# Kernel tuning notes

Measured on AMD Instinct MI355X. Metric: run time of the kernel, lower is better.

The kernel has to match this reference:

```python
import jax, jax.numpy as jnp
from jax import lax
import numpy as np

K = 3  # kernel size for both convs


def setup_inputs() -> dict:
    key = jax.random.key(0)
    k1, k2, k3, k4, k5 = jax.random.split(key, 5)
    x = jax.random.normal(k1, (8, 3, 384, 384), dtype=jnp.float32)
    # offset-producing conv: 18 = 2*3*3 offset channels for a 3x3 deform kernel
    w1 = jax.random.normal(k2, (18, 3, K, K), dtype=jnp.float32) * 0.05
    b1 = jax.random.normal(k3, (18,), dtype=jnp.float32) * 0.05
    # deformable conv weight/bias: in=3, out=3, 3x3
    w2 = jax.random.normal(k4, (3, 3, K, K), dtype=jnp.float32) * 0.2
    b2 = jax.random.normal(k5, (3,), dtype=jnp.float32) * 0.05
    return {"x": x, "w1": w1, "b1": b1, "w2": w2, "b2": b2}


def _deform_conv2d(x, offset, w, b):
    # x: [B,C,H,W], offset: [B, 2*K*K, Ho, Wo] (per-tap (dy,dx) interleaved),
    # w: [Co,C,K,K], b: [Co]. stride=1, pad=0, dilation=1, zero-padding bilinear.
    B, C, H, W = x.shape
    KK = K * K
    Ho, Wo = H - (K - 1), W - (K - 1)
    off = offset.reshape(B, KK, 2, Ho, Wo)
    dy, dx = off[:, :, 0], off[:, :, 1]                      # [B,KK,Ho,Wo]

    kh = jnp.repeat(jnp.arange(K, dtype=jnp.float32), K)     # [KK] kernel row
    kw = jnp.tile(jnp.arange(K, dtype=jnp.float32), K)       # [KK] kernel col
    base_y = jnp.arange(Ho, dtype=jnp.float32)[None, :, None] + kh[:, None, None]  # [KK,Ho,1]
    base_x = jnp.arange(Wo, dtype=jnp.float32)[None, None, :] + kw[:, None, None]  # [KK,1,Wo]
    py = base_y[None] + dy                                   # [B,KK,Ho,Wo]
    px = base_x[None] + dx

    y0 = jnp.floor(py)
    x0 = jnp.floor(px)
    wy = py - y0
    wx = px - x0

    x_flat = x.reshape(B, C, H * W)
    N = KK * Ho * Wo

    def gather_corner(yc, xc, wgt):
        valid = (yc >= 0) & (yc <= H - 1) & (xc >= 0) & (xc <= W - 1)
        yi = jnp.clip(yc, 0, H - 1).astype(jnp.int32)
        xi = jnp.clip(xc, 0, W - 1).astype(jnp.int32)
        idx = (yi * W + xi).reshape(B, 1, N)
        g = jnp.take_along_axis(x_flat, idx, axis=2)          # [B,C,N]
        return g * (wgt * valid.astype(x.dtype)).reshape(B, 1, N)

    val = gather_corner(y0, x0, (1 - wy) * (1 - wx))
    val = val + gather_corner(y0, x0 + 1, (1 - wy) * wx)
    val = val + gather_corner(y0 + 1, x0, wy * (1 - wx))
    val = val + gather_corner(y0 + 1, x0 + 1, wy * wx)
    val = val.reshape(B, C, KK, Ho, Wo)

    out = jnp.einsum('bckhw,ock->bohw', val, w.reshape(w.shape[0], C, KK))
    return out + b[None, :, None, None]


def reference(x, w1, b1, w2, b2):
    offset = lax.conv_general_dilated(
        x, w1, window_strides=(1, 1), padding='VALID',
        dimension_numbers=('NCHW', 'OIHW', 'NCHW')) + b1[None, :, None, None]
    return _deform_conv2d(x, offset, w2, b2)
```

## Files before the change

### kernel.cpp

```cpp
#include <hip/hip_runtime.h>


#define BB 8
#define HH 384
#define WW 384
#define HO 382
#define WO 382
#define HW (HH * WW)
#define TW 32
#define TH 8
#define TILES_X 12
#define TILES_Y 48
#define SROWS 15
#define SCOLS 39
#define SSTRIDE 39

typedef float v2f __attribute__((ext_vector_type(2), aligned(4)));
typedef float v4f __attribute__((ext_vector_type(4), aligned(16)));

static __device__ __forceinline__ v2f fma2(v2f a, v2f b, v2f c) {
    return __builtin_elementwise_fma(a, b, c);
}
static __device__ __forceinline__ v4f fma4(v4f a, v4f b, v4f c) {
    return __builtin_elementwise_fma(a, b, c);
}

__global__ __launch_bounds__(256) void deform_tiled(
    const float* __restrict__ x,
    const float* __restrict__ w1,
    const float* __restrict__ b1,
    const float* __restrict__ w2,
    const float* __restrict__ b2,
    float* __restrict__ out)
{
    __shared__ v4f  s_tile[SROWS * SSTRIDE];
    __shared__ float s_w1p[486];
    __shared__ float s_b1[18];
    __shared__ float s_w2p[54];
    __shared__ float s_w2s[27];
    __shared__ float s_b2[3];

    for (int i = threadIdx.x; i < 486; i += 256) {
        const int oc = i / 27, rem = i % 27, c = rem / 9, j = rem % 9;
        const int k = oc >> 1, comp = oc & 1;
        s_w1p[((j * 3 + c) * 9 + k) * 2 + comp] = w1[i];
    }
    if (threadIdx.x < 81) {
        const int i = threadIdx.x;
        const int o = i / 27, c = (i % 27) / 9, k = i % 9;
        if (o < 2) s_w2p[(k * 3 + c) * 2 + o] = w2[i];
        else       s_w2s[k * 3 + c] = w2[i];
    }
    if (threadIdx.x < 18) s_b1[threadIdx.x] = b1[threadIdx.x];
    if (threadIdx.x < 3)  s_b2[threadIdx.x] = b2[threadIdx.x];

    const int b  = blockIdx.x & 7;
    const int t  = blockIdx.x >> 3;
    const int tx = t % TILES_X;
    const int ty = t / TILES_X;
    const int w0 = tx * TW;
    const int r0 = ty * TH;

    const float* xp0 = x + (long)b * 3 * HW;
    const float* xp1 = xp0 + HW;
    const float* xp2 = xp0 + 2 * HW;

    const int gr0 = r0 - 2, gc0 = w0 - 2;
    for (int s = threadIdx.x; s < SROWS * SCOLS; s += 256) {
        const int sr = s / SCOLS, sc = s - sr * SCOLS;
        const int gy = min(max(gr0 + sr, 0), HH - 1);
        const int gx = min(max(gc0 + sc, 0), WW - 1);
        const int base = gy * WW + gx;
        v4f v;
        v.x = xp0[base];
        v.y = xp1[base];
        v.z = xp2[base];
        v.w = 0.f;
        s_tile[sr * SSTRIDE + sc] = v;
    }
    __syncthreads();

    const int wo_in = threadIdx.x & 31;
    const int ho_in = threadIdx.x >> 5;
    const int wo = w0 + wo_in;
    const int ho = r0 + ho_in;
    if (wo >= WO || ho >= HO) return;

    v2f off2[9];
#pragma unroll
    for (int k = 0; k < 9; ++k) {
        v2f v; v.x = s_b1[2 * k]; v.y = s_b1[2 * k + 1];
        off2[k] = v;
    }

    const v2f* w1p = (const v2f*)s_w1p;
#pragma unroll
    for (int j = 0; j < 9; ++j) {
        const int i = j / 3, jj = j % 3;
        const v4f q = s_tile[(ho_in + 2 + i) * SSTRIDE + (wo_in + 2 + jj)];
#pragma unroll
        for (int c = 0; c < 3; ++c) {
            const float xc = (c == 0) ? q.x : (c == 1) ? q.y : q.z;
            v2f xcv; xcv.x = xc; xcv.y = xc;
            const v2f* wrow = w1p + (j * 3 + c) * 9;
#pragma unroll
            for (int k = 0; k < 9; ++k)
                off2[k] = fma2(xcv, wrow[k], off2[k]);
        }
    }

    float acc0 = s_b2[0], acc1 = s_b2[1], acc2 = s_b2[2];
    const v2f* w2p = (const v2f*)s_w2p;

    const bool interior = (gr0 >= 0) & (gc0 >= 0) &
                          (gr0 + SROWS <= HH) & (gc0 + SCOLS <= WW);

    if (interior) {
        unsigned bad = 0u;
#pragma unroll
        for (int k = 0; k < 9; ++k) {
            const int kh = k / 3, kw = k - kh * 3;
            v2f pos; pos.x = (float)(ho + kh); pos.y = (float)(wo + kw);
            pos += off2[k];
            const v2f fl = __builtin_elementwise_floor(pos);
            const v2f fr = pos - fl;
            const int y0 = (int)fl.x;
            const int x0 = (int)fl.y;
            const int ly0 = y0 - gr0;
            const int lx  = x0 - gc0;

            bad |= (((unsigned)ly0 > (unsigned)(SROWS - 2)) |
                    ((unsigned)lx  > (unsigned)(SCOLS - 2))) ? (1u << k) : 0u;

            const float g00 = (1.f - fr.x) * (1.f - fr.y);
            const float g01 = (1.f - fr.x) * fr.y;
            const float g10 = fr.x * (1.f - fr.y);
            const float g11 = fr.x * fr.y;

            const int cy0 = min(max(ly0, 0), SROWS - 2);
            const int cx  = min(max(lx, 0),  SCOLS - 2);
            const v4f* p0 = s_tile + cy0 * SSTRIDE + cx;
            const v4f* p1 = p0 + SSTRIDE;
            const v4f q00 = p0[0], q01 = p0[1];
            const v4f q10 = p1[0], q11 = p1[1];

            v4f gv; gv.x = g00; gv.y = g00; gv.z = g00; gv.w = g00;
            v4f t4 = gv * q00;
            gv.x = g01; gv.y = g01; gv.z = g01; gv.w = g01;
            t4 = fma4(gv, q01, t4);
            gv.x = g10; gv.y = g10; gv.z = g10; gv.w = g10;
            t4 = fma4(gv, q10, t4);
            gv.x = g11; gv.y = g11; gv.z = g11; gv.w = g11;
            t4 = fma4(gv, q11, t4);

            const float v0 = t4.x, v1 = t4.y, v2v = t4.z;

            v2f acc01; acc01.x = acc0; acc01.y = acc1;
            v2f vv;
            vv.x = v0;  vv.y = v0;  acc01 = fma2(vv, w2p[k * 3 + 0], acc01);
            vv.x = v1;  vv.y = v1;  acc01 = fma2(vv, w2p[k * 3 + 1], acc01);
            vv.x = v2v; vv.y = v2v; acc01 = fma2(vv, w2p[k * 3 + 2], acc01);
            acc0 = acc01.x; acc1 = acc01.y;
            acc2 = fmaf(s_w2s[k * 3 + 0], v0, acc2);
            acc2 = fmaf(s_w2s[k * 3 + 1], v1, acc2);
            acc2 = fmaf(s_w2s[k * 3 + 2], v2v, acc2);
        }

        if (bad) {
#pragma unroll 1
            for (int k = 0; k < 9; ++k) {
                if ((bad >> k) & 1u) {
                    const int kh = k / 3, kw = k - kh * 3;
                    v2f pos; pos.x = (float)(ho + kh); pos.y = (float)(wo + kw);
                    pos += off2[k];
                    const v2f fl = __builtin_elementwise_floor(pos);
                    const v2f fr = pos - fl;
                    const int y0 = (int)fl.x;
                    const int x0 = (int)fl.y;

                    const int ly0 = y0 - gr0;
                    const int lx  = x0 - gc0;
                    const float a00 = (1.f - fr.x) * (1.f - fr.y);
                    const float a01 = (1.f - fr.x) * fr.y;
                    const float a10 = fr.x * (1.f - fr.y);
                    const float a11 = fr.x * fr.y;
                    const int cy0 = min(max(ly0, 0), SROWS - 2);
                    const int cx  = min(max(lx, 0),  SCOLS - 2);
                    const v4f* p0 = s_tile + cy0 * SSTRIDE + cx;
                    const v4f* p1 = p0 + SSTRIDE;
                    const v4f w00v = p0[0], w01v = p0[1];
                    const v4f w10v = p1[0], w11v = p1[1];
                    v4f gv; gv.x = a00; gv.y = a00; gv.z = a00; gv.w = a00;
                    v4f tw = gv * w00v;
                    gv.x = a01; gv.y = a01; gv.z = a01; gv.w = a01;
                    tw = fma4(gv, w01v, tw);
                    gv.x = a10; gv.y = a10; gv.z = a10; gv.w = a10;
                    tw = fma4(gv, w10v, tw);
                    gv.x = a11; gv.y = a11; gv.z = a11; gv.w = a11;
                    tw = fma4(gv, w11v, tw);

                    const int ry0 = min(max(y0, 0), HH - 1);
                    const int ry1 = min(max(y0 + 1, 0), HH - 1);
                    const int xbs = min(max(x0, 0), WW - 2);
                    const bool vy0 = (y0 >= 0) & (y0 <= HH - 1);
                    const bool vy1 = (y0 >= -1) & (y0 <= HH - 2);
                    const bool vx0 = (x0 >= 0) & (x0 <= WW - 1);
                    const bool vx1 = (x0 >= -1) & (x0 <= WW - 2);
                    const float wy0m = vy0 ? (1.f - fr.x) : 0.f;
                    const float wy1m = vy1 ? fr.x : 0.f;
                    const float wx0m = vx0 ? (1.f - fr.y) : 0.f;
                    const float wx1m = vx1 ? fr.y : 0.f;
                    const bool selA = (x0 >= WW - 1);
                    const bool selB = (x0 >= 0);
                    const float e0 = (selA ? 0.f : wx0m) + (selB ? 0.f : wx1m);
                    const float e1 = (selA ? wx0m : 0.f) + (selB ? wx1m : 0.f);
                    const float g00 = wy0m * e0, g01 = wy0m * e1;
                    const float g10 = wy1m * e0, g11 = wy1m * e1;
                    const int o0 = ry0 * WW + xbs;
                    const int o1 = ry1 * WW + xbs;
                    v4f q00, q01, q10, q11;
                    q00.x = xp0[o0];     q00.y = xp1[o0];     q00.z = xp2[o0];     q00.w = 0.f;
                    q01.x = xp0[o0 + 1]; q01.y = xp1[o0 + 1]; q01.z = xp2[o0 + 1]; q01.w = 0.f;
                    q10.x = xp0[o1];     q10.y = xp1[o1];     q10.z = xp2[o1];     q10.w = 0.f;
                    q11.x = xp0[o1 + 1]; q11.y = xp1[o1 + 1]; q11.z = xp2[o1 + 1]; q11.w = 0.f;
                    gv.x = g00; gv.y = g00; gv.z = g00; gv.w = g00;
                    v4f tr = gv * q00;
                    gv.x = g01; gv.y = g01; gv.z = g01; gv.w = g01;
                    tr = fma4(gv, q01, tr);
                    gv.x = g10; gv.y = g10; gv.z = g10; gv.w = g10;
                    tr = fma4(gv, q10, tr);
                    gv.x = g11; gv.y = g11; gv.z = g11; gv.w = g11;
                    tr = fma4(gv, q11, tr);

                    const float d0 = tr.x - tw.x;
                    const float d1 = tr.y - tw.y;
                    const float d2 = tr.z - tw.z;

                    v2f acc01; acc01.x = acc0; acc01.y = acc1;
                    v2f vv;
                    vv.x = d0; vv.y = d0; acc01 = fma2(vv, w2p[k * 3 + 0], acc01);
                    vv.x = d1; vv.y = d1; acc01 = fma2(vv, w2p[k * 3 + 1], acc01);
                    vv.x = d2; vv.y = d2; acc01 = fma2(vv, w2p[k * 3 + 2], acc01);
                    acc0 = acc01.x; acc1 = acc01.y;
                    acc2 = fmaf(s_w2s[k * 3 + 0], d0, acc2);
                    acc2 = fmaf(s_w2s[k * 3 + 1], d1, acc2);
                    acc2 = fmaf(s_w2s[k * 3 + 2], d2, acc2);
                }
            }
        }
    } else {
#pragma unroll 1
        for (int k = 0; k < 9; ++k) {
            const int kh = k / 3, kw = k - kh * 3;
            v2f pos; pos.x = (float)(ho + kh); pos.y = (float)(wo + kw);
            pos += off2[k];
            const v2f fl = __builtin_elementwise_floor(pos);
            const v2f fr = pos - fl;
            const int y0 = (int)fl.x;
            const int x0 = (int)fl.y;

            const int ry0 = min(max(y0, 0), HH - 1);
            const int ry1 = min(max(y0 + 1, 0), HH - 1);
            const int xbs = min(max(x0, 0), WW - 2);

            const bool vy0 = (y0 >= 0) & (y0 <= HH - 1);
            const bool vy1 = (y0 >= -1) & (y0 <= HH - 2);
            const bool vx0 = (x0 >= 0) & (x0 <= WW - 1);
            const bool vx1 = (x0 >= -1) & (x0 <= WW - 2);
            const float wy0m = vy0 ? (1.f - fr.x) : 0.f;
            const float wy1m = vy1 ? fr.x : 0.f;
            const float wx0m = vx0 ? (1.f - fr.y) : 0.f;
            const float wx1m = vx1 ? fr.y : 0.f;

            const bool selA = (x0 >= WW - 1);
            const bool selB = (x0 >= 0);
            const float e0 = (selA ? 0.f : wx0m) + (selB ? 0.f : wx1m);
            const float e1 = (selA ? wx0m : 0.f) + (selB ? wx1m : 0.f);
            const float g00 = wy0m * e0, g01 = wy0m * e1;
            const float g10 = wy1m * e0, g11 = wy1m * e1;

            const int ly0 = ry0 - gr0;
            const int ly1 = ry1 - gr0;
            const int lx  = xbs - gc0;
            const bool inTile = ((unsigned)ly0 <= SROWS - 1) &
                                ((unsigned)ly1 <= SROWS - 1) &
                                ((unsigned)lx  <= SCOLS - 2);

            const int cy0 = min(max(ly0, 0), SROWS - 1);
            const int cy1 = min(max(ly1, 0), SROWS - 1);
            const int cx  = min(max(lx, 0),  SCOLS - 2);
            const v4f* p0 = s_tile + cy0 * SSTRIDE + cx;
            const v4f* p1 = s_tile + cy1 * SSTRIDE + cx;
            v4f q00 = p0[0], q01 = p0[1];
            v4f q10 = p1[0], q11 = p1[1];

            if (!inTile) {
                const int o0 = ry0 * WW + xbs;
                const int o1 = ry1 * WW + xbs;
                q00.x = xp0[o0];     q00.y = xp1[o0];     q00.z = xp2[o0];
                q01.x = xp0[o0 + 1]; q01.y = xp1[o0 + 1]; q01.z = xp2[o0 + 1];
                q10.x = xp0[o1];     q10.y = xp1[o1];     q10.z = xp2[o1];
                q11.x = xp0[o1 + 1]; q11.y = xp1[o1 + 1]; q11.z = xp2[o1 + 1];
            }

            v4f gv; gv.x = g00; gv.y = g00; gv.z = g00; gv.w = g00;
            v4f t4 = gv * q00;
            gv.x = g01; gv.y = g01; gv.z = g01; gv.w = g01;
            t4 = fma4(gv, q01, t4);
            gv.x = g10; gv.y = g10; gv.z = g10; gv.w = g10;
            t4 = fma4(gv, q10, t4);
            gv.x = g11; gv.y = g11; gv.z = g11; gv.w = g11;
            t4 = fma4(gv, q11, t4);

            const float v0 = t4.x, v1 = t4.y, v2v = t4.z;

            v2f acc01; acc01.x = acc0; acc01.y = acc1;
            v2f vv;
            vv.x = v0;  vv.y = v0;  acc01 = fma2(vv, w2p[k * 3 + 0], acc01);
            vv.x = v1;  vv.y = v1;  acc01 = fma2(vv, w2p[k * 3 + 1], acc01);
            vv.x = v2v; vv.y = v2v; acc01 = fma2(vv, w2p[k * 3 + 2], acc01);
            acc0 = acc01.x; acc1 = acc01.y;
            acc2 = fmaf(s_w2s[k * 3 + 0], v0, acc2);
            acc2 = fmaf(s_w2s[k * 3 + 1], v1, acc2);
            acc2 = fmaf(s_w2s[k * 3 + 2], v2v, acc2);
        }
    }

    const long obase = ((long)(b * 3) * HO + ho) * WO + wo;
    __builtin_nontemporal_store(acc0, out + obase);
    __builtin_nontemporal_store(acc1, out + obase + (long)HO * WO);
    __builtin_nontemporal_store(acc2, out + obase + 2L * HO * WO);
}

extern "C" void kernel_launch(void* const* d_in, const int* in_sizes, int n_in,
                              void* d_out, int out_size, void* d_ws, size_t ws_size,
                              hipStream_t stream) {
    const float* x  = (const float*)d_in[0];
    const float* w1 = (const float*)d_in[1];
    const float* b1 = (const float*)d_in[2];
    const float* w2 = (const float*)d_in[3];
    const float* b2 = (const float*)d_in[4];
    float* out = (float*)d_out;

    const int blocks = TILES_X * TILES_Y * BB;
    deform_tiled<<<blocks, 256, 0, stream>>>(x, w1, b1, w2, b2, out);
}
```

Before: 109.6 us.

## Widen tiles to 64x8 with 512 threads and unify interior/border paths

Doubles the tile width to 64 output columns and uses 512-thread blocks, which cuts the halo overhead of the shared-memory tile and halves the block count. The separate interior and border code paths are merged into one fast path. It uses a bad-tap bitmask that now also checks image bounds, and a corrective slow path handles those taps. This reduces code size and divergence between block types, at the cost of larger shared memory per block and possibly lower occupancy.

```diff
diff --git a/kernel.cpp b/kernel.cpp
--- a/kernel.cpp
+++ b/kernel.cpp
@@ -7,13 +7,14 @@
 #define HO 382
 #define WO 382
 #define HW (HH * WW)
-#define TW 32
+#define TW 64
 #define TH 8
-#define TILES_X 12
+#define TILES_X 6
 #define TILES_Y 48
 #define SROWS 15
-#define SCOLS 39
-#define SSTRIDE 39
+#define SCOLS 71
+#define SSTRIDE 71
+#define NTHREADS 512
 
 typedef float v2f __attribute__((ext_vector_type(2), aligned(4)));
 typedef float v4f __attribute__((ext_vector_type(4), aligned(16)));
@@ -25,7 +26,7 @@
     return __builtin_elementwise_fma(a, b, c);
 }
 
-__global__ __launch_bounds__(256) void deform_tiled(
+__global__ __launch_bounds__(NTHREADS) void deform_tiled(
     const float* __restrict__ x,
     const float* __restrict__ w1,
     const float* __restrict__ b1,
@@ -40,7 +41,8 @@
     __shared__ float s_w2s[27];
     __shared__ float s_b2[3];
 
-    for (int i = threadIdx.x; i < 486; i += 256) {
+    if (threadIdx.x < 486) {
+        const int i = threadIdx.x;
         const int oc = i / 27, rem = i % 27, c = rem / 9, j = rem % 9;
         const int k = oc >> 1, comp = oc & 1;
         s_w1p[((j * 3 + c) * 9 + k) * 2 + comp] = w1[i];
@@ -66,7 +68,7 @@
     const float* xp2 = xp0 + 2 * HW;
 
     const int gr0 = r0 - 2, gc0 = w0 - 2;
-    for (int s = threadIdx.x; s < SROWS * SCOLS; s += 256) {
+    for (int s = threadIdx.x; s < SROWS * SCOLS; s += NTHREADS) {
         const int sr = s / SCOLS, sc = s - sr * SCOLS;
         const int gy = min(max(gr0 + sr, 0), HH - 1);
         const int gx = min(max(gc0 + sc, 0), WW - 1);
@@ -80,8 +82,8 @@
     }
     __syncthreads();
 
-    const int wo_in = threadIdx.x & 31;
-    const int ho_in = threadIdx.x >> 5;
+    const int wo_in = threadIdx.x & 63;
+    const int ho_in = threadIdx.x >> 6;
     const int wo = w0 + wo_in;
     const int ho = r0 + ho_in;
     if (wo >= WO || ho >= HO) return;
@@ -112,217 +114,139 @@
     float acc0 = s_b2[0], acc1 = s_b2[1], acc2 = s_b2[2];
     const v2f* w2p = (const v2f*)s_w2p;
 
-    const bool interior = (gr0 >= 0) & (gc0 >= 0) &
-                          (gr0 + SROWS <= HH) & (gc0 + SCOLS <= WW);
-
-    if (interior) {
-        unsigned bad = 0u;
-#pragma unroll
-        for (int k = 0; k < 9; ++k) {
-            const int kh = k / 3, kw = k - kh * 3;
-            v2f pos; pos.x = (float)(ho + kh); pos.y = (float)(wo + kw);
-            pos += off2[k];
-            const v2f fl = __builtin_elementwise_floor(pos);
-            const v2f fr = pos - fl;
-            const int y0 = (int)fl.x;
-            const int x0 = (int)fl.y;
-            const int ly0 = y0 - gr0;
-            const int lx  = x0 - gc0;
-
-            bad |= (((unsigned)ly0 > (unsigned)(SROWS - 2)) |
-                    ((unsigned)lx  > (unsigned)(SCOLS - 2))) ? (1u << k) : 0u;
-
-            const float g00 = (1.f - fr.x) * (1.f - fr.y);
-            const float g01 = (1.f - fr.x) * fr.y;
-            const float g10 = fr.x * (1.f - fr.y);
-            const float g11 = fr.x * fr.y;
-
-            const int cy0 = min(max(ly0, 0), SROWS - 2);
-            const int cx  = min(max(lx, 0),  SCOLS - 2);
-            const v4f* p0 = s_tile + cy0 * SSTRIDE + cx;
-            const v4f* p1 = p0 + SSTRIDE;
-            const v4f q00 = p0[0], q01 = p0[1];
-            const v4f q10 = p1[0], q11 = p1[1];
-
-            v4f gv; gv.x = g00; gv.y = g00; gv.z = g00; gv.w = g00;
-            v4f t4 = gv * q00;
-            gv.x = g01; gv.y = g01; gv.z = g01; gv.w = g01;
-            t4 = fma4(gv, q01, t4);
-            gv.x = g10; gv.y = g10; gv.z = g10; gv.w = g10;
-            t4 = fma4(gv, q10, t4);
-            gv.x = g11; gv.y = g11; gv.z = g11; gv.w = g11;
-            t4 = fma4(gv, q11, t4);
-
-            const float v0 = t4.x, v1 = t4.y, v2v = t4.z;
-
-            v2f acc01; acc01.x = acc0; acc01.y = acc1;
-            v2f vv;
-            vv.x = v0;  vv.y = v0;  acc01 = fma2(vv, w2p[k * 3 + 0], acc01);
-            vv.x = v1;  vv.y = v1;  acc01 = fma2(vv, w2p[k * 3 + 1], acc01);
-            vv.x = v2v; vv.y = v2v; acc01 = fma2(vv, w2p[k * 3 + 2], acc01);
-            acc0 = acc01.x; acc1 = acc01.y;
-            acc2 = fmaf(s_w2s[k * 3 + 0], v0, acc2);
-            acc2 = fmaf(s_w2s[k * 3 + 1], v1, acc2);
-            acc2 = fmaf(s_w2s[k * 3 + 2], v2v, acc2);
-        }
-
-        if (bad) {
-#pragma unroll 1
-            for (int k = 0; k < 9; ++k) {
-                if ((bad >> k) & 1u) {
-                    const int kh = k / 3, kw = k - kh * 3;
-                    v2f pos; pos.x = (float)(ho + kh); pos.y = (float)(wo + kw);
-                    pos += off2[k];
-                    const v2f fl = __builtin_elementwise_floor(pos);
-                    const v2f fr = pos - fl;
-                    const int y0 = (int)fl.x;
-                    const int x0 = (int)fl.y;
-
-                    const int ly0 = y0 - gr0;
-                    const int lx  = x0 - gc0;
-                    const float a00 = (1.f - fr.x) * (1.f - fr.y);
-                    const float a01 = (1.f - fr.x) * fr.y;
-                    const float a10 = fr.x * (1.f - fr.y);
-                    const float a11 = fr.x * fr.y;
-                    const int cy0 = min(max(ly0, 0), SROWS - 2);
-                    const int cx  = min(max(lx, 0),  SCOLS - 2);
-                    const v4f* p0 = s_tile + cy0 * SSTRIDE + cx;
-                    const v4f* p1 = p0 + SSTRIDE;
-                    const v4f w00v = p0[0], w01v = p0[1];
-                    const v4f w10v = p1[0], w11v = p1[1];
-                    v4f gv; gv.x = a00; gv.y = a00; gv.z = a00; gv.w = a00;
-                    v4f tw = gv * w00v;
-                    gv.x = a01; gv.y = a01; gv.z = a01; gv.w = a01;
-                    tw = fma4(gv, w01v, tw);
-                    gv.x = a10; gv.y = a10; gv.z = a10; gv.w = a10;
-                    tw = fma4(gv, w10v, tw);
-                    gv.x = a11; gv.y = a11; gv.z = a11; gv.w = a11;
-                    tw = fma4(gv, w11v, tw);
-
-                    const int ry0 = min(max(y0, 0), HH - 1);
-                    const int ry1 = min(max(y0 + 1, 0), HH - 1);
-                    const int xbs = min(max(x0, 0), WW - 2);
-                    const bool vy0 = (y0 >= 0) & (y0 <= HH - 1);
-                    const bool vy1 = (y0 >= -1) & (y0 <= HH - 2);
-                    const bool vx0 = (x0 >= 0) & (x0 <= WW - 1);
-                    const bool vx1 = (x0 >= -1) & (x0 <= WW - 2);
-                    const float wy0m = vy0 ? (1.f - fr.x) : 0.f;
-                    const float wy1m = vy1 ? fr.x : 0.f;
-                    const float wx0m = vx0 ? (1.f - fr.y) : 0.f;
-                    const float wx1m = vx1 ? fr.y : 0.f;
-                    const bool selA = (x0 >= WW - 1);
-                    const bool selB = (x0 >= 0);
-                    const float e0 = (selA ? 0.f : wx0m) + (selB ? 0.f : wx1m);
-                    const float e1 = (selA ? wx0m : 0.f) + (selB ? wx1m : 0.f);
-                    const float g00 = wy0m * e0, g01 = wy0m * e1;
-                    const float g10 = wy1m * e0, g11 = wy1m * e1;
-                    const int o0 = ry0 * WW + xbs;
-                    const int o1 = ry1 * WW + xbs;
-                    v4f q00, q01, q10, q11;
-                    q00.x = xp0[o0];     q00.y = xp1[o0];     q00.z = xp2[o0];     q00.w = 0.f;
-                    q01.x = xp0[o0 + 1]; q01.y = xp1[o0 + 1]; q01.z = xp2[o0 + 1]; q01.w = 0.f;
-                    q10.x = xp0[o1];     q10.y = xp1[o1];     q10.z = xp2[o1];     q10.w = 0.f;
-                    q11.x = xp0[o1 + 1]; q11.y = xp1[o1 + 1]; q11.z = xp2[o1 + 1]; q11.w = 0.f;
-                    gv.x = g00; gv.y = g00; gv.z = g00; gv.w = g00;
-                    v4f tr = gv * q00;
-                    gv.x = g01; gv.y = g01; gv.z = g01; gv.w = g01;
-                    tr = fma4(gv, q01, tr);
-                    gv.x = g10; gv.y = g10; gv.z = g10; gv.w = g10;
-                    tr = fma4(gv, q10, tr);
-                    gv.x = g11; gv.y = g11; gv.z = g11; gv.w = g11;
-                    tr = fma4(gv, q11, tr);
-
-                    const float d0 = tr.x - tw.x;
-                    const float d1 = tr.y - tw.y;
-                    const float d2 = tr.z - tw.z;
-
-                    v2f acc01; acc01.x = acc0; acc01.y = acc1;
-                    v2f vv;
-                    vv.x = d0; vv.y = d0; acc01 = fma2(vv, w2p[k * 3 + 0], acc01);
-                    vv.x = d1; vv.y = d1; acc01 = fma2(vv, w2p[k * 3 + 1], acc01);
-                    vv.x = d2; vv.y = d2; acc01 = fma2(vv, w2p[k * 3 + 2], acc01);
-                    acc0 = acc01.x; acc1 = acc01.y;
-                    acc2 = fmaf(s_w2s[k * 3 + 0], d0, acc2);
-                    acc2 = fmaf(s_w2s[k * 3 + 1], d1, acc2);
-                    acc2 = fmaf(s_w2s[k * 3 + 2], d2, acc2);
-                }
-            }
-        }
-    } else {
+    unsigned bad = 0u;
+#pragma unroll
+    for (int k = 0; k < 9; ++k) {
+        const int kh = k / 3, kw = k - kh * 3;
+        v2f pos; pos.x = (float)(ho + kh); pos.y = (float)(wo + kw);
+        pos += off2[k];
+        const v2f fl = __builtin_elementwise_floor(pos);
+        const v2f fr = pos - fl;
+        const int y0 = (int)fl.x;
+        const int x0 = (int)fl.y;
+        const int ly0 = y0 - gr0;
+        const int lx  = x0 - gc0;
+
+        const bool ok = ((unsigned)y0 <= (unsigned)(HH - 2)) &
+                        ((unsigned)x0 <= (unsigned)(WW - 2)) &
+                        ((unsigned)ly0 <= (unsigned)(SROWS - 2)) &
+                        ((unsigned)lx  <= (unsigned)(SCOLS - 2));
+        bad |= ok ? 0u : (1u << k);
+
+        const float g00 = (1.f - fr.x) * (1.f - fr.y);
+        const float g01 = (1.f - fr.x) * fr.y;
+        const float g10 = fr.x * (1.f - fr.y);
+        const float g11 = fr.x * fr.y;
+
+        const int cy0 = min(max(ly0, 0), SROWS - 2);
+        const int cx  = min(max(lx, 0),  SCOLS - 2);
+        const v4f* p0 = s_tile + cy0 * SSTRIDE + cx;
+        const v4f* p1 = p0 + SSTRIDE;
+        const v4f q00 = p0[0], q01 = p0[1];
+        const v4f q10 = p1[0], q11 = p1[1];
+
+        v4f gv; gv.x = g00; gv.y = g00; gv.z = g00; gv.w = g00;
+        v4f t4 = gv * q00;
+        gv.x = g01; gv.y = g01; gv.z = g01; gv.w = g01;
+        t4 = fma4(gv, q01, t4);
+        gv.x = g10; gv.y = g10; gv.z = g10; gv.w = g10;
+        t4 = fma4(gv, q10, t4);
+        gv.x = g11; gv.y = g11; gv.z = g11; gv.w = g11;
+        t4 = fma4(gv, q11, t4);
+
+        const float v0 = t4.x, v1 = t4.y, v2v = t4.z;
+
+        v2f acc01; acc01.x = acc0; acc01.y = acc1;
+        v2f vv;
+        vv.x = v0;  vv.y = v0;  acc01 = fma2(vv, w2p[k * 3 + 0], acc01);
+        vv.x = v1;  vv.y = v1;  acc01 = fma2(vv, w2p[k * 3 + 1], acc01);
+        vv.x = v2v; vv.y = v2v; acc01 = fma2(vv, w2p[k * 3 + 2], acc01);
+        acc0 = acc01.x; acc1 = acc01.y;
+        acc2 = fmaf(s_w2s[k * 3 + 0], v0, acc2);
+        acc2 = fmaf(s_w2s[k * 3 + 1], v1, acc2);
+        acc2 = fmaf(s_w2s[k * 3 + 2], v2v, acc2);
+    }
+
+    if (bad) {
 #pragma unroll 1
         for (int k = 0; k < 9; ++k) {
-            const int kh = k / 3, kw = k - kh * 3;
-            v2f pos; pos.x = (float)(ho + kh); pos.y = (float)(wo + kw);
-            pos += off2[k];
-            const v2f fl = __builtin_elementwise_floor(pos);
-            const v2f fr = pos - fl;
-            const int y0 = (int)fl.x;
-            const int x0 = (int)fl.y;
-
-            const int ry0 = min(max(y0, 0), HH - 1);
-            const int ry1 = min(max(y0 + 1, 0), HH - 1);
-            const int xbs = min(max(x0, 0), WW - 2);
-
-            const bool vy0 = (y0 >= 0) & (y0 <= HH - 1);
-            const bool vy1 = (y0 >= -1) & (y0 <= HH - 2);
-            const bool vx0 = (x0 >= 0) & (x0 <= WW - 1);
-            const bool vx1 = (x0 >= -1) & (x0 <= WW - 2);
-            const float wy0m = vy0 ? (1.f - fr.x) : 0.f;
-            const float wy1m = vy1 ? fr.x : 0.f;
-            const float wx0m = vx0 ? (1.f - fr.y) : 0.f;
-            const float wx1m = vx1 ? fr.y : 0.f;
-
-            const bool selA = (x0 >= WW - 1);
-            const bool selB = (x0 >= 0);
-            const float e0 = (selA ? 0.f : wx0m) + (selB ? 0.f : wx1m);
-            const float e1 = (selA ? wx0m : 0.f) + (selB ? wx1m : 0.f);
-            const float g00 = wy0m * e0, g01 = wy0m * e1;
-            const float g10 = wy1m * e0, g11 = wy1m * e1;
-
-            const int ly0 = ry0 - gr0;
-            const int ly1 = ry1 - gr0;
-            const int lx  = xbs - gc0;
-            const bool inTile = ((unsigned)ly0 <= SROWS - 1) &
-                                ((unsigned)ly1 <= SROWS - 1) &
-                                ((unsigned)lx  <= SCOLS - 2);
-
-            const int cy0 = min(max(ly0, 0), SROWS - 1);
-            const int cy1 = min(max(ly1, 0), SROWS - 1);
-            const int cx  = min(max(lx, 0),  SCOLS - 2);
-            const v4f* p0 = s_tile + cy0 * SSTRIDE + cx;
-            const v4f* p1 = s_tile + cy1 * SSTRIDE + cx;
-            v4f q00 = p0[0], q01 = p0[1];
-            v4f q10 = p1[0], q11 = p1[1];
-
-            if (!inTile) {
+            if ((bad >> k) & 1u) {
+                const int kh = k / 3, kw = k - kh * 3;
+                v2f pos; pos.x = (float)(ho + kh); pos.y = (float)(wo + kw);
+                pos += off2[k];
+                const v2f fl = __builtin_elementwise_floor(pos);
+                const v2f fr = pos - fl;
+                const int y0 = (int)fl.x;
+                const int x0 = (int)fl.y;
+
+                const int ly0 = y0 - gr0;
+                const int lx  = x0 - gc0;
+                const float a00 = (1.f - fr.x) * (1.f - fr.y);
+                const float a01 = (1.f - fr.x) * fr.y;
+                const float a10 = fr.x * (1.f - fr.y);
+                const float a11 = fr.x * fr.y;
+                const int cy0 = min(max(ly0, 0), SROWS - 2);
+                const int cx  = min(max(lx, 0),  SCOLS - 2);
+                const v4f* p0 = s_tile + cy0 * SSTRIDE + cx;
+                const v4f* p1 = p0 + SSTRIDE;
+                const v4f w00v = p0[0], w01v = p0[1];
+                const v4f w10v = p1[0], w11v = p1[1];
+                v4f gv; gv.x = a00; gv.y = a00; gv.z = a00; gv.w = a00;
+                v4f tw = gv * w00v;
+                gv.x = a01; gv.y = a01; gv.z = a01; gv.w = a01;
+                tw = fma4(gv, w01v, tw);
+                gv.x = a10; gv.y = a10; gv.z = a10; gv.w = a10;
+                tw = fma4(gv, w10v, tw);
+                gv.x = a11; gv.y = a11; gv.z = a11; gv.w = a11;
+                tw = fma4(gv, w11v, tw);
+
+                const int ry0 = min(max(y0, 0), HH - 1);
+                const int ry1 = min(max(y0 + 1, 0), HH - 1);
+                const int xbs = min(max(x0, 0), WW - 2);
+                const bool vy0 = (y0 >= 0) & (y0 <= HH - 1);
+                const bool vy1 = (y0 >= -1) & (y0 <= HH - 2);
+                const bool vx0 = (x0 >= 0) & (x0 <= WW - 1);
+                const bool vx1 = (x0 >= -1) & (x0 <= WW - 2);
+                const float wy0m = vy0 ? (1.f - fr.x) : 0.f;
+                const float wy1m = vy1 ? fr.x : 0.f;
+                const float wx0m = vx0 ? (1.f - fr.y) : 0.f;
+                const float wx1m = vx1 ? fr.y : 0.f;
+                const bool selA = (x0 >= WW - 1);
+                const bool selB = (x0 >= 0);
+                const float e0 = (selA ? 0.f : wx0m) + (selB ? 0.f : wx1m);
+                const float e1 = (selA ? wx0m : 0.f) + (selB ? wx1m : 0.f);
+                const float g00 = wy0m * e0, g01 = wy0m * e1;
+                const float g10 = wy1m * e0, g11 = wy1m * e1;
                 const int o0 = ry0 * WW + xbs;
                 const int o1 = ry1 * WW + xbs;
-                q00.x = xp0[o0];     q00.y = xp1[o0];     q00.z = xp2[o0];
-                q01.x = xp0[o0 + 1]; q01.y = xp1[o0 + 1]; q01.z = xp2[o0 + 1];
-                q10.x = xp0[o1];     q10.y = xp1[o1];     q10.z = xp2[o1];
-                q11.x = xp0[o1 + 1]; q11.y = xp1[o1 + 1]; q11.z = xp2[o1 + 1];
+                v4f q00, q01, q10, q11;
+                q00.x = xp0[o0];     q00.y = xp1[o0];     q00.z = xp2[o0];     q00.w = 0.f;
+                q01.x = xp0[o0 + 1]; q01.y = xp1[o0 + 1]; q01.z = xp2[o0 + 1]; q01.w = 0.f;
+                q10.x = xp0[o1];     q10.y = xp1[o1];     q10.z = xp2[o1];     q10.w = 0.f;
+                q11.x = xp0[o1 + 1]; q11.y = xp1[o1 + 1]; q11.z = xp2[o1 + 1]; q11.w = 0.f;
+                gv.x = g00; gv.y = g00; gv.z = g00; gv.w = g00;
+                v4f tr = gv * q00;
+                gv.x = g01; gv.y = g01; gv.z = g01; gv.w = g01;
+                tr = fma4(gv, q01, tr);
+                gv.x = g10; gv.y = g10; gv.z = g10; gv.w = g10;
+                tr = fma4(gv, q10, tr);
+                gv.x = g11; gv.y = g11; gv.z = g11; gv.w = g11;
+                tr = fma4(gv, q11, tr);
+
+                const float d0 = tr.x - tw.x;
+                const float d1 = tr.y - tw.y;
+                const float d2 = tr.z - tw.z;
+
+                v2f acc01; acc01.x = acc0; acc01.y = acc1;
+                v2f vv;
+                vv.x = d0; vv.y = d0; acc01 = fma2(vv, w2p[k * 3 + 0], acc01);
+                vv.x = d1; vv.y = d1; acc01 = fma2(vv, w2p[k * 3 + 1], acc01);
+                vv.x = d2; vv.y = d2; acc01 = fma2(vv, w2p[k * 3 + 2], acc01);
+                acc0 = acc01.x; acc1 = acc01.y;
+                acc2 = fmaf(s_w2s[k * 3 + 0], d0, acc2);
+                acc2 = fmaf(s_w2s[k * 3 + 1], d1, acc2);
+                acc2 = fmaf(s_w2s[k * 3 + 2], d2, acc2);
             }
-
-            v4f gv; gv.x = g00; gv.y = g00; gv.z = g00; gv.w = g00;
-            v4f t4 = gv * q00;
-            gv.x = g01; gv.y = g01; gv.z = g01; gv.w = g01;
-            t4 = fma4(gv, q01, t4);
-            gv.x = g10; gv.y = g10; gv.z = g10; gv.w = g10;
-            t4 = fma4(gv, q10, t4);
-            gv.x = g11; gv.y = g11; gv.z = g11; gv.w = g11;
-            t4 = fma4(gv, q11, t4);
-
-            const float v0 = t4.x, v1 = t4.y, v2v = t4.z;
-
-            v2f acc01; acc01.x = acc0; acc01.y = acc1;
-            v2f vv;
-            vv.x = v0;  vv.y = v0;  acc01 = fma2(vv, w2p[k * 3 + 0], acc01);
-            vv.x = v1;  vv.y = v1;  acc01 = fma2(vv, w2p[k * 3 + 1], acc01);
-            vv.x = v2v; vv.y = v2v; acc01 = fma2(vv, w2p[k * 3 + 2], acc01);
-            acc0 = acc01.x; acc1 = acc01.y;
-            acc2 = fmaf(s_w2s[k * 3 + 0], v0, acc2);
-            acc2 = fmaf(s_w2s[k * 3 + 1], v1, acc2);
-            acc2 = fmaf(s_w2s[k * 3 + 2], v2v, acc2);
         }
     }
 
@@ -343,5 +267,5 @@
     float* out = (float*)d_out;
 
     const int blocks = TILES_X * TILES_Y * BB;
-    deform_tiled<<<blocks, 256, 0, stream>>>(x, w1, b1, w2, b2, out);
-}
+    deform_tiled<<<blocks, NTHREADS, 0, stream>>>(x, w1, b1, w2, b2, out);
+}
```

After: 112.3 us. +2.4%, slower.
